# Kernel optimization log

Measured on AMD Instinct MI355X. Metric: run time of the kernel, lower is better.

Reference implementation:

```python
import jax, jax.numpy as jnp
import numpy as np

CUTOFF = 8.0
NUM_G = 50
HID = 128
NUM_INTER = 3
NUM_NODES = 50000
NUM_EDGES = 1600000
NUM_GRAPHS = 128
MAX_Z = 100
LOG2 = float(np.log(2.0))


def ssp(x):
    # PyG ShiftedSoftplus
    return jax.nn.softplus(x) - LOG2


def setup_inputs() -> dict:
    key = jax.random.key(0)
    ks = jax.random.split(key, 20)
    s = 0.1
    pos = jax.random.normal(ks[0], (NUM_NODES, 3), dtype=jnp.float32) * 4.0
    edge_shift = jax.random.normal(ks[1], (NUM_EDGES, 3), dtype=jnp.float32) * 0.5
    z = jax.random.randint(ks[2], (NUM_NODES,), 0, MAX_Z, dtype=jnp.int32)
    edge_index = jax.random.randint(ks[3], (2, NUM_EDGES), 0, NUM_NODES, dtype=jnp.int32)
    batch = jnp.sort(jax.random.randint(ks[4], (NUM_NODES,), 0, NUM_GRAPHS, dtype=jnp.int32))
    emb = jax.random.normal(ks[5], (MAX_Z, HID), dtype=jnp.float32) * s
    mlp_w1 = jax.random.normal(ks[6], (NUM_INTER, NUM_G, HID), dtype=jnp.float32) * s
    mlp_b1 = jnp.zeros((NUM_INTER, HID), jnp.float32)
    mlp_w2 = jax.random.normal(ks[7], (NUM_INTER, HID, HID), dtype=jnp.float32) * s
    mlp_b2 = jnp.zeros((NUM_INTER, HID), jnp.float32)
    cf_w1 = jax.random.normal(ks[8], (NUM_INTER, HID, HID), dtype=jnp.float32) * s  # no bias (PyG lin1)
    cf_w2 = jax.random.normal(ks[9], (NUM_INTER, HID, HID), dtype=jnp.float32) * s
    cf_b2 = jnp.zeros((NUM_INTER, HID), jnp.float32)
    lin_w = jax.random.normal(ks[10], (NUM_INTER, HID, HID), dtype=jnp.float32) * s
    lin_b = jnp.zeros((NUM_INTER, HID), jnp.float32)
    head_w1 = jax.random.normal(ks[11], (HID, HID // 2), dtype=jnp.float32) * s
    head_b1 = jnp.zeros((HID // 2,), jnp.float32)
    head_w2 = jax.random.normal(ks[12], (HID // 2, 1), dtype=jnp.float32) * s
    head_b2 = jnp.zeros((1,), jnp.float32)
    return dict(pos=pos, edge_shift=edge_shift, emb=emb, mlp_w1=mlp_w1, mlp_b1=mlp_b1,
                mlp_w2=mlp_w2, mlp_b2=mlp_b2, cf_w1=cf_w1, cf_w2=cf_w2, cf_b2=cf_b2,
                lin_w=lin_w, lin_b=lin_b, head_w1=head_w1, head_b1=head_b1,
                head_w2=head_w2, head_b2=head_b2, z=z, edge_index=edge_index, batch=batch)


def reference(pos, edge_shift, emb, mlp_w1, mlp_b1, mlp_w2, mlp_b2, cf_w1, cf_w2, cf_b2,
              lin_w, lin_b, head_w1, head_b1, head_w2, head_b2, z, edge_index, batch):
    src, dst = edge_index[0], edge_index[1]
    # edge distances: pos[row] - (pos[col] + shift)
    rel = pos[src] - (pos[dst] + edge_shift)            # [E,3]
    w = jnp.linalg.norm(rel, axis=-1)                   # [E]
    # Gaussian smearing
    offset = jnp.linspace(0.0, CUTOFF, NUM_G, dtype=pos.dtype)
    coeff = -0.5 / (offset[1] - offset[0]) ** 2
    edge_attr = jnp.exp(coeff * (w[:, None] - offset) ** 2)   # [E,50]
    # cosine cutoff
    C = 0.5 * (jnp.cos(w * jnp.pi / CUTOFF) + 1.0)            # [E]
    h = emb[z]                                                # [N,128]
    for i in range(NUM_INTER):
        Wf = (ssp(edge_attr @ mlp_w1[i] + mlp_b1[i]) @ mlp_w2[i] + mlp_b2[i]) * C[:, None]  # [E,128]
        msg = (h @ cf_w1[i])[src] * Wf                   # gather-multiply  [E,128]
        agg = jax.ops.segment_sum(msg, dst, num_segments=NUM_NODES)         # scatter-sum [N,128]
        h = h + (ssp(agg @ cf_w2[i] + cf_b2[i]) @ lin_w[i] + lin_b[i])
    out_atom = ssp(h @ head_w1 + head_b1) @ head_w2 + head_b2               # [N,1]
    sums = jax.ops.segment_sum(out_atom, batch, num_segments=NUM_GRAPHS)    # [G,1]
    counts = jax.ops.segment_sum(jnp.ones((NUM_NODES, 1), out_atom.dtype), batch, num_segments=NUM_GRAPHS)
    return sums / jnp.maximum(counts, 1.0)  # mean readout; out_proj is Identity (128==128)
```

## Files before the change

kernel.cpp:

```cpp
#include <hip/hip_runtime.h>
#include <hip/hip_fp16.h>
#include <math.h>

#define NNODES  50000
#define NEDGES  1600000
#define NGRAPHS 128
#define HID     128
#define NG      50
#define NITER   3
#define TPTS    2048
#define WMAX    12.0f
#define PI_F    3.14159265358979323846f

typedef __attribute__((ext_vector_type(4))) _Float16 half4;
typedef __attribute__((ext_vector_type(4))) float   f32x4;

__device__ __forceinline__ float ssp(float x) {
    float sp = fmaxf(x, 0.0f) + log1pf(expf(-fabsf(x)));
    return sp - 0.69314718055994530942f;
}

__global__ __launch_bounds__(256) void k_init_h(const float* __restrict__ emb,
                                                const int* __restrict__ z,
                                                float* __restrict__ h,
                                                _Float16* __restrict__ hH)
{
    int idx = blockIdx.x * 256 + threadIdx.x;
    int n = idx >> 7, c = idx & 127;
    float v = emb[(z[n] << 7) + c];
    h[idx] = v;
    hH[idx] = (_Float16)v;
}

__global__ __launch_bounds__(128) void k_wt(const float* __restrict__ in,
                                            _Float16* __restrict__ out)
{
    int it = blockIdx.x >> 7, c = blockIdx.x & 127, j = threadIdx.x;
    out[(size_t)it * 16384 + c * 128 + j] = (_Float16)in[(size_t)it * 16384 + j * 128 + c];
}

__global__ __launch_bounds__(128) void k_table(const float* __restrict__ W1,
                                               const float* __restrict__ B1,
                                               const float* __restrict__ W2,
                                               const float* __restrict__ B2,
                                               __half* __restrict__ ti)
{
    int it = blockIdx.x / TPTS;
    int pt = blockIdx.x - it * TPTS;
    const float* W1i = W1 + (size_t)it * NG * HID;
    const float* B1i = B1 + (size_t)it * HID;
    const float* W2i = W2 + (size_t)it * HID * HID;
    const float* B2i = B2 + (size_t)it * HID;

    const float step = WMAX / (float)(TPTS - 1);
    float w0 = pt * step;
    int ptn = (pt < TPTS - 1) ? pt + 1 : pt;
    float w1v = ptn * step;

    __shared__ float sEA[2][NG];
    __shared__ float sT1[2][HID];
    int k = threadIdx.x;
    {
        float dx = 8.0f / 49.0f;
        float coeff = -0.5f / (dx * dx);
        if (k < NG) {
            float diff = w0 - (float)k * dx;
            sEA[0][k] = expf(coeff * diff * diff);
        } else if (k >= 64 && k < 64 + NG) {
            float diff = w1v - (float)(k - 64) * dx;
            sEA[1][k - 64] = expf(coeff * diff * diff);
        }
    }
    __syncthreads();
    float a0 = B1i[k], a1 = a0;
    for (int g = 0; g < NG; ++g) {
        float wv = W1i[g * HID + k];
        a0 = fmaf(sEA[0][g], wv, a0);
        a1 = fmaf(sEA[1][g], wv, a1);
    }
    sT1[0][k] = ssp(a0);
    sT1[1][k] = ssp(a1);
    __syncthreads();
    float b0 = B2i[k], b1v = b0;
    for (int j = 0; j < HID; ++j) {
        float wv = W2i[j * HID + k];
        b0  = fmaf(sT1[0][j], wv, b0);
        b1v = fmaf(sT1[1][j], wv, b1v);
    }
    size_t base = ((size_t)it * TPTS + pt) * 256;
    int pair = k >> 1, within = k & 1;
    ti[base + pair * 4 + within]     = __float2half(b0);
    ti[base + pair * 4 + within + 2] = __float2half(b1v - b0);
}

__global__ __launch_bounds__(256) void k_hist(const int* __restrict__ ei,
                                              int* __restrict__ deg)
{
    int e = blockIdx.x * 256 + threadIdx.x;
    if (e >= NEDGES) return;
    atomicAdd(&deg[ei[NEDGES + e]], 1);
}

#define SCAN_T 1024
#define CHUNK  49
__global__ __launch_bounds__(SCAN_T) void k_scan(const int* __restrict__ deg,
                                                 int* __restrict__ rowptr,
                                                 int* __restrict__ cursor)
{
    int tid = threadIdx.x;
    int base = tid * CHUNK;
    int vals[CHUNK];
    int local = 0;
    #pragma unroll
    for (int i = 0; i < CHUNK; ++i) {
        int idx = base + i;
        int v = (idx < NNODES) ? deg[idx] : 0;
        vals[i] = local;
        local += v;
    }
    int lane = tid & 63, wid = tid >> 6;
    int x = local;
    #pragma unroll
    for (int off = 1; off < 64; off <<= 1) {
        int y = __shfl_up(x, off);
        if (lane >= off) x += y;
    }
    __shared__ int wsum[16];
    __shared__ int woff[17];
    if (lane == 63) wsum[wid] = x;
    __syncthreads();
    if (tid == 0) {
        int acc = 0;
        #pragma unroll
        for (int i = 0; i < 16; ++i) { woff[i] = acc; acc += wsum[i]; }
        woff[16] = acc;
    }
    __syncthreads();
    int threadExcl = woff[wid] + x - local;
    #pragma unroll
    for (int i = 0; i < CHUNK; ++i) {
        int idx = base + i;
        if (idx < NNODES) {
            int p = threadExcl + vals[i];
            rowptr[idx] = p;
            cursor[idx] = p;
        }
    }
    if (tid == SCAN_T - 1) rowptr[NNODES] = woff[16];
}

__global__ __launch_bounds__(256) void k_scatter(const int* __restrict__ ei,
                                                 const float* __restrict__ pos,
                                                 const float* __restrict__ shift,
                                                 int* __restrict__ cursor,
                                                 uint2* __restrict__ rec)
{
    int e = blockIdx.x * 256 + threadIdx.x;
    if (e >= NEDGES) return;
    int s = ei[e], d = ei[NEDGES + e];
    float rx = pos[3*s+0] - (pos[3*d+0] + shift[3*e+0]);
    float ry = pos[3*s+1] - (pos[3*d+1] + shift[3*e+1]);
    float rz = pos[3*s+2] - (pos[3*d+2] + shift[3*e+2]);
    float w = sqrtf(rx*rx + ry*ry + rz*rz);
    const float SCALE = (float)(TPTS - 1) / WMAX;
    float t = fminf(w * SCALE, (float)(TPTS - 1));
    int i0 = (int)t; if (i0 > TPTS - 2) i0 = TPTS - 2;
    float fr = t - (float)i0;
    float C = 0.5f * (cosf(w * (PI_F / 8.0f)) + 1.0f);
    __half2 frc = __halves2half2(__float2half(fr), __float2half(C));
    int slot = atomicAdd(&cursor[d], 1);
    rec[slot] = make_uint2((unsigned)s | ((unsigned)i0 << 17), *(unsigned*)&frc);
}

__device__ __forceinline__ void edge_contrib(uint2 rv, int lane,
                                             const char* __restrict__ hfBase,
                                             const char* __restrict__ tbBase,
                                             float& ax, float& ay)
{
    unsigned sB = (rv.x & 0x1FFFFu) << 8;
    unsigned tB = (rv.x >> 17) << 9;
    __half2 frc = *reinterpret_cast<__half2*>(&rv.y);
    __half2 fr2 = __half2half2(__low2half(frc));
    __half2 c2  = __half2half2(__high2half(frc));
    uint2 tv = *reinterpret_cast<const uint2*>(tbBase + tB + lane * 8);
    unsigned hu = *reinterpret_cast<const unsigned*>(hfBase + sB + lane * 4);
    __half2 hv   = *reinterpret_cast<__half2*>(&hu);
    __half2 vals = *reinterpret_cast<__half2*>(&tv.x);
    __half2 dels = *reinterpret_cast<__half2*>(&tv.y);
    __half2 f2 = __hfma2(fr2, dels, vals);
    __half2 ch = __hmul2(c2, hv);
    ax = fmaf(__low2float(f2),  __low2float(ch),  ax);
    ay = fmaf(__high2float(f2), __high2float(ch), ay);
}

__global__ __launch_bounds__(256) void k_gather(const uint2* __restrict__ rec,
                                                const int* __restrict__ rowptr,
                                                const __half* __restrict__ hfH,
                                                const __half* __restrict__ tableH,
                                                __half2* __restrict__ aggH)
{
    int node = blockIdx.x * 4 + (threadIdx.x >> 6);
    int lane = threadIdx.x & 63;
    const char* hfBase = (const char*)hfH;
    const char* tbBase = (const char*)tableH;
    int beg = rowptr[node], end = rowptr[node + 1];
    float ax0 = 0.f, ay0 = 0.f, ax1 = 0.f, ay1 = 0.f;
    int k = beg;
    for (; k + 4 <= end; k += 4) {
        uint2 r0 = rec[k], r1 = rec[k+1], r2 = rec[k+2], r3 = rec[k+3];
        edge_contrib(r0, lane, hfBase, tbBase, ax0, ay0);
        edge_contrib(r1, lane, hfBase, tbBase, ax1, ay1);
        edge_contrib(r2, lane, hfBase, tbBase, ax0, ay0);
        edge_contrib(r3, lane, hfBase, tbBase, ax1, ay1);
    }
    for (; k < end; ++k) edge_contrib(rec[k], lane, hfBase, tbBase, ax0, ay0);
    aggH[(size_t)node * 64 + lane] = __floats2half2_rn(ax0 + ax1, ay0 + ay1);
}

__global__ __launch_bounds__(256) void k_ngemm_mfma(const _Float16* __restrict__ hH,
                                                    const _Float16* __restrict__ Wt,
                                                    _Float16* __restrict__ outH)
{
    int tid = threadIdx.x;
    int wave = tid >> 6, l = tid & 63;
    int lr = l & 15, lg = l >> 4;
    int r0 = blockIdx.x * 16;
    f32x4 acc[2];
    acc[0] = (f32x4){0.f, 0.f, 0.f, 0.f};
    acc[1] = (f32x4){0.f, 0.f, 0.f, 0.f};
    const _Float16* aRow = hH + (size_t)(r0 + lr) * HID;
    #pragma unroll
    for (int kk = 0; kk < 8; ++kk) {
        half4 a = *(const half4*)(aRow + kk * 16 + lg * 4);
        #pragma unroll
        for (int c = 0; c < 2; ++c) {
            int ct = wave * 2 + c;
            half4 b = *(const half4*)(Wt + (size_t)(ct * 16 + lr) * HID + kk * 16 + lg * 4);
            acc[c] = __builtin_amdgcn_mfma_f32_16x16x16f16(a, b, acc[c], 0, 0, 0);
        }
    }
    #pragma unroll
    for (int c = 0; c < 2; ++c) {
        int col = (wave * 2 + c) * 16 + lr;
        #pragma unroll
        for (int r = 0; r < 4; ++r)
            outH[(size_t)(r0 + lg * 4 + r) * HID + col] = (_Float16)acc[c][r];
    }
}

__global__ __launch_bounds__(256) void k_update_mfma(const _Float16* __restrict__ aggH,
                                                     const _Float16* __restrict__ W2t,
                                                     const float* __restrict__ B2,
                                                     const _Float16* __restrict__ Lt,
                                                     const float* __restrict__ LB,
                                                     float* __restrict__ h,
                                                     _Float16* __restrict__ hH)
{
    __shared__ _Float16 sT[16 * 128];
    int tid = threadIdx.x;
    int wave = tid >> 6, l = tid & 63;
    int lr = l & 15, lg = l >> 4;
    int r0 = blockIdx.x * 16;

    f32x4 acc[2];
    acc[0] = (f32x4){0.f, 0.f, 0.f, 0.f};
    acc[1] = (f32x4){0.f, 0.f, 0.f, 0.f};
    const _Float16* aRow = aggH + (size_t)(r0 + lr) * HID;
    #pragma unroll
    for (int kk = 0; kk < 8; ++kk) {
        half4 a = *(const half4*)(aRow + kk * 16 + lg * 4);
        #pragma unroll
        for (int c = 0; c < 2; ++c) {
            int ct = wave * 2 + c;
            half4 b = *(const half4*)(W2t + (size_t)(ct * 16 + lr) * HID + kk * 16 + lg * 4);
            acc[c] = __builtin_amdgcn_mfma_f32_16x16x16f16(a, b, acc[c], 0, 0, 0);
        }
    }
    #pragma unroll
    for (int c = 0; c < 2; ++c) {
        int col = (wave * 2 + c) * 16 + lr;
        float bias = B2[col];
        #pragma unroll
        for (int r = 0; r < 4; ++r) {
            int rl = lg * 4 + r;
            float v = ssp(acc[c][r] + bias);
            int byte = rl * 256 + col * 2;
            byte ^= (rl & 7) << 4;
            *(_Float16*)((char*)sT + byte) = (_Float16)v;
        }
    }
    __syncthreads();
    f32x4 acc2[2];
    acc2[0] = (f32x4){0.f, 0.f, 0.f, 0.f};
    acc2[1] = (f32x4){0.f, 0.f, 0.f, 0.f};
    #pragma unroll
    for (int kk = 0; kk < 8; ++kk) {
        int byte = lr * 256 + (kk * 16 + lg * 4) * 2;
        byte ^= (lr & 7) << 4;
        half4 a = *(const half4*)((char*)sT + byte);
        #pragma unroll
        for (int c = 0; c < 2; ++c) {
            int ct = wave * 2 + c;
            half4 b = *(const half4*)(Lt + (size_t)(ct * 16 + lr) * HID + kk * 16 + lg * 4);
            acc2[c] = __builtin_amdgcn_mfma_f32_16x16x16f16(a, b, acc2[c], 0, 0, 0);
        }
    }
    #pragma unroll
    for (int c = 0; c < 2; ++c) {
        int col = (wave * 2 + c) * 16 + lr;
        float lb = LB[col];
        #pragma unroll
        for (int r = 0; r < 4; ++r) {
            int row = r0 + lg * 4 + r;
            float hv = h[(size_t)row * HID + col] + acc2[c][r] + lb;
            h[(size_t)row * HID + col] = hv;
            hH[(size_t)row * HID + col] = (_Float16)hv;
        }
    }
}

__global__ __launch_bounds__(512) void k_head(const float* __restrict__ h,
                                              const float* __restrict__ w1,
                                              const float* __restrict__ b1,
                                              const float* __restrict__ w2,
                                              const float* __restrict__ b2,
                                              const int* __restrict__ batch,
                                              float* __restrict__ sums_pad)
{
    __shared__ float sA[128 * 132];
    int r0 = blockIdx.x * 128;
    int tid = threadIdx.x;
    for (int idx = tid; idx < 128 * 32; idx += 512) {
        int r = idx >> 5, c4 = idx & 31;
        int row = r0 + r;
        float4 v = make_float4(0.f, 0.f, 0.f, 0.f);
        if (row < NNODES) v = *(const float4*)(h + (size_t)row * HID + c4 * 4);
        *(float4*)(&sA[r * 132 + c4 * 4]) = v;
    }
    __syncthreads();
    int tx = tid & 7, ty = tid >> 3;
    int cc = tx * 8, ee = ty * 2;
    float acc[2][8];
    {
        float4 b0 = *(const float4*)(b1 + cc);
        float4 bb = *(const float4*)(b1 + cc + 4);
        #pragma unroll
        for (int e = 0; e < 2; ++e) {
            acc[e][0]=b0.x; acc[e][1]=b0.y; acc[e][2]=b0.z; acc[e][3]=b0.w;
            acc[e][4]=bb.x; acc[e][5]=bb.y; acc[e][6]=bb.z; acc[e][7]=bb.w;
        }
    }
    #pragma unroll 4
    for (int j = 0; j < HID; ++j) {
        float a0 = sA[(ee + 0) * 132 + j];
        float a1 = sA[(ee + 1) * 132 + j];
        float4 w0 = *(const float4*)(w1 + (size_t)j * 64 + cc);
        float4 wv1 = *(const float4*)(w1 + (size_t)j * 64 + cc + 4);
        float wv[8] = {w0.x,w0.y,w0.z,w0.w,wv1.x,wv1.y,wv1.z,wv1.w};
        #pragma unroll
        for (int c = 0; c < 8; ++c) {
            acc[0][c] = fmaf(a0, wv[c], acc[0][c]);
            acc[1][c] = fmaf(a1, wv[c], acc[1][c]);
        }
    }
    float4 w2a = *(const float4*)(w2 + cc);
    float4 w2b = *(const float4*)(w2 + cc + 4);
    float w2v[8] = {w2a.x,w2a.y,w2a.z,w2a.w,w2b.x,w2b.y,w2b.z,w2b.w};
    float bias2 = b2[0];
    #pragma unroll
    for (int e = 0; e < 2; ++e) {
        float part = 0.f;
        #pragma unroll
        for (int c = 0; c < 8; ++c) part = fmaf(ssp(acc[e][c]), w2v[c], part);
        part += __shfl_down(part, 4, 8);
        part += __shfl_down(part, 2, 8);
        part += __shfl_down(part, 1, 8);
        if (tx == 0) {
            int row = r0 + ee + e;
            if (row < NNODES) {
                int b = batch[row];
                atomicAdd(&sums_pad[b * 16], part + bias2);
            }
        }
    }
}

__global__ void k_final(const float* __restrict__ sums_pad,
                        const int* __restrict__ batch,
                        float* __restrict__ out)
{
    int g = threadIdx.x;
    if (g >= NGRAPHS) return;
    int lo = 0, hi = NNODES;
    while (lo < hi) { int mid = (lo + hi) >> 1; if (batch[mid] < g) lo = mid + 1; else hi = mid; }
    int a = lo;
    lo = 0; hi = NNODES;
    while (lo < hi) { int mid = (lo + hi) >> 1; if (batch[mid] < g + 1) lo = mid + 1; else hi = mid; }
    float cnt = (float)(lo - a);
    out[g] = sums_pad[g * 16] / fmaxf(cnt, 1.0f);
}

extern "C" void kernel_launch(void* const* d_in, const int* in_sizes, int n_in,
                              void* d_out, int out_size, void* d_ws, size_t ws_size,
                              hipStream_t stream)
{
    const float* pos     = (const float*)d_in[0];
    const float* shift   = (const float*)d_in[1];
    const float* emb     = (const float*)d_in[2];
    const float* mlp_w1  = (const float*)d_in[3];
    const float* mlp_b1  = (const float*)d_in[4];
    const float* mlp_w2  = (const float*)d_in[5];
    const float* mlp_b2  = (const float*)d_in[6];
    const float* cf_w1   = (const float*)d_in[7];
    const float* cf_w2   = (const float*)d_in[8];
    const float* cf_b2   = (const float*)d_in[9];
    const float* lin_w   = (const float*)d_in[10];
    const float* lin_b   = (const float*)d_in[11];
    const float* head_w1 = (const float*)d_in[12];
    const float* head_b1 = (const float*)d_in[13];
    const float* head_w2 = (const float*)d_in[14];
    const float* head_b2 = (const float*)d_in[15];
    const int*   z       = (const int*)d_in[16];
    const int*   ei      = (const int*)d_in[17];
    const int*   batch   = (const int*)d_in[18];
    float* out = (float*)d_out;

    float* ws = (float*)d_ws;
    size_t off = 0;
    float*    h       = ws + off; off += (size_t)NNODES * HID;
    _Float16* hH      = (_Float16*)(ws + off); off += (size_t)(NNODES + 64) * HID / 2;
    _Float16* hfH     = (_Float16*)(ws + off); off += (size_t)(NNODES + 64) * HID / 2;
    _Float16* aggH    = (_Float16*)(ws + off); off += (size_t)(NNODES + 64) * HID / 2;
    __half*   tableH  = (__half*)(ws + off); off += (size_t)3 * TPTS * 256 / 2;
    _Float16* w1t     = (_Float16*)(ws + off); off += (size_t)3 * HID * HID / 2;
    _Float16* w2t     = (_Float16*)(ws + off); off += (size_t)3 * HID * HID / 2;
    _Float16* lwt     = (_Float16*)(ws + off); off += (size_t)3 * HID * HID / 2;
    uint2*    rec     = (uint2*)(ws + off); off += (size_t)2 * NEDGES;
    int*      rowptr  = (int*)(ws + off); off += NNODES + 1;
    int*      deg     = (int*)(ws + off); off += NNODES;
    int*      cursor  = (int*)(ws + off); off += NNODES;
    float*    sums_pad= ws + off; off += NGRAPHS * 16;

    hipMemsetAsync(deg, 0, NNODES * sizeof(int), stream);
    hipMemsetAsync(sums_pad, 0, NGRAPHS * 16 * sizeof(float), stream);

    k_hist<<<(NEDGES + 255) / 256, 256, 0, stream>>>(ei, deg);
    k_scan<<<1, SCAN_T, 0, stream>>>(deg, rowptr, cursor);
    k_scatter<<<(NEDGES + 255) / 256, 256, 0, stream>>>(ei, pos, shift, cursor, rec);

    k_init_h<<<NNODES * HID / 256, 256, 0, stream>>>(emb, z, h, hH);
    k_table<<<3 * TPTS, 128, 0, stream>>>(mlp_w1, mlp_b1, mlp_w2, mlp_b2, tableH);
    k_wt<<<3 * 128, 128, 0, stream>>>(cf_w1, w1t);
    k_wt<<<3 * 128, 128, 0, stream>>>(cf_w2, w2t);
    k_wt<<<3 * 128, 128, 0, stream>>>(lin_w, lwt);

    int gblk = NNODES / 16;
    for (int i = 0; i < NITER; ++i) {
        k_ngemm_mfma<<<gblk, 256, 0, stream>>>(hH, w1t + (size_t)i * HID * HID, hfH);
        k_gather<<<NNODES / 4, 256, 0, stream>>>(rec, rowptr, (const __half*)hfH,
                                                 tableH + (size_t)i * TPTS * 256,
                                                 (__half2*)aggH);
        k_update_mfma<<<gblk, 256, 0, stream>>>(aggH, w2t + (size_t)i * HID * HID,
                                                cf_b2 + (size_t)i * HID,
                                                lwt + (size_t)i * HID * HID,
                                                lin_b + (size_t)i * HID, h, hH);
    }
    k_head<<<(NNODES + 127) / 128, 512, 0, stream>>>(h, head_w1, head_b1, head_w2, head_b2, batch, sums_pad);
    k_final<<<1, 128, 0, stream>>>(sums_pad, batch, out);
}
```

Baseline: 1.016 ms.

## Fuse next-layer node GEMM into update kernel, vectorize gather record loads

The update kernel now also multiplies the freshly updated h tile by the next interaction's cf_w1 and writes hfH, so two of the three separate node-GEMM launches and their re-read of hH are removed. The gather kernel loads edge records as 16-byte nontemporal vectors and processes eight edges per iteration, with an alignment prologue and tail handling. The three weight-transpose launches are merged into one. The fused update adds an extra shared-memory pass and barrier per block, and raises register pressure.

Result: no change. 1.018 ms (+0.2%).

```diff
diff --git a/kernel.cpp b/kernel.cpp
--- a/kernel.cpp
+++ b/kernel.cpp
@@ -14,6 +14,7 @@
 
 typedef __attribute__((ext_vector_type(4))) _Float16 half4;
 typedef __attribute__((ext_vector_type(4))) float   f32x4;
+typedef __attribute__((ext_vector_type(4))) unsigned u32x4;
 
 __device__ __forceinline__ float ssp(float x) {
     float sp = fmaxf(x, 0.0f) + log1pf(expf(-fabsf(x)));
@@ -32,10 +33,18 @@
     hH[idx] = (_Float16)v;
 }
 
-__global__ __launch_bounds__(128) void k_wt(const float* __restrict__ in,
-                                            _Float16* __restrict__ out)
-{
-    int it = blockIdx.x >> 7, c = blockIdx.x & 127, j = threadIdx.x;
+__global__ __launch_bounds__(128) void k_wt3(const float* __restrict__ w1,
+                                             const float* __restrict__ w2,
+                                             const float* __restrict__ lw,
+                                             _Float16* __restrict__ o1,
+                                             _Float16* __restrict__ o2,
+                                             _Float16* __restrict__ o3)
+{
+    int fam = blockIdx.x / 384;
+    int rem = blockIdx.x - fam * 384;
+    int it = rem >> 7, c = rem & 127, j = threadIdx.x;
+    const float* in = (fam == 0) ? w1 : (fam == 1) ? w2 : lw;
+    _Float16* out   = (fam == 0) ? o1 : (fam == 1) ? o2 : o3;
     out[(size_t)it * 16384 + c * 128 + j] = (_Float16)in[(size_t)it * 16384 + j * 128 + c];
 }
 
@@ -172,14 +181,14 @@
     rec[slot] = make_uint2((unsigned)s | ((unsigned)i0 << 17), *(unsigned*)&frc);
 }
 
-__device__ __forceinline__ void edge_contrib(uint2 rv, int lane,
+__device__ __forceinline__ void edge_contrib(unsigned rx, unsigned ry, int lane,
                                              const char* __restrict__ hfBase,
                                              const char* __restrict__ tbBase,
                                              float& ax, float& ay)
 {
-    unsigned sB = (rv.x & 0x1FFFFu) << 8;
-    unsigned tB = (rv.x >> 17) << 9;
-    __half2 frc = *reinterpret_cast<__half2*>(&rv.y);
+    unsigned sB = (rx & 0x1FFFFu) << 8;
+    unsigned tB = (rx >> 17) << 9;
+    __half2 frc = *reinterpret_cast<__half2*>(&ry);
     __half2 fr2 = __half2half2(__low2half(frc));
     __half2 c2  = __half2half2(__high2half(frc));
     uint2 tv = *reinterpret_cast<const uint2*>(tbBase + tB + lane * 8);
@@ -206,14 +215,34 @@
     int beg = rowptr[node], end = rowptr[node + 1];
     float ax0 = 0.f, ay0 = 0.f, ax1 = 0.f, ay1 = 0.f;
     int k = beg;
-    for (; k + 4 <= end; k += 4) {
-        uint2 r0 = rec[k], r1 = rec[k+1], r2 = rec[k+2], r3 = rec[k+3];
-        edge_contrib(r0, lane, hfBase, tbBase, ax0, ay0);
-        edge_contrib(r1, lane, hfBase, tbBase, ax1, ay1);
-        edge_contrib(r2, lane, hfBase, tbBase, ax0, ay0);
-        edge_contrib(r3, lane, hfBase, tbBase, ax1, ay1);
-    }
-    for (; k < end; ++k) edge_contrib(rec[k], lane, hfBase, tbBase, ax0, ay0);
+    if ((k & 1) && k < end) {
+        uint2 r = rec[k];
+        edge_contrib(r.x, r.y, lane, hfBase, tbBase, ax0, ay0);
+        ++k;
+    }
+    for (; k + 8 <= end; k += 8) {
+        u32x4 ra = __builtin_nontemporal_load(reinterpret_cast<const u32x4*>(rec + k));
+        u32x4 rb = __builtin_nontemporal_load(reinterpret_cast<const u32x4*>(rec + k + 2));
+        u32x4 rc = __builtin_nontemporal_load(reinterpret_cast<const u32x4*>(rec + k + 4));
+        u32x4 rd = __builtin_nontemporal_load(reinterpret_cast<const u32x4*>(rec + k + 6));
+        edge_contrib(ra.x, ra.y, lane, hfBase, tbBase, ax0, ay0);
+        edge_contrib(ra.z, ra.w, lane, hfBase, tbBase, ax1, ay1);
+        edge_contrib(rb.x, rb.y, lane, hfBase, tbBase, ax0, ay0);
+        edge_contrib(rb.z, rb.w, lane, hfBase, tbBase, ax1, ay1);
+        edge_contrib(rc.x, rc.y, lane, hfBase, tbBase, ax0, ay0);
+        edge_contrib(rc.z, rc.w, lane, hfBase, tbBase, ax1, ay1);
+        edge_contrib(rd.x, rd.y, lane, hfBase, tbBase, ax0, ay0);
+        edge_contrib(rd.z, rd.w, lane, hfBase, tbBase, ax1, ay1);
+    }
+    for (; k + 2 <= end; k += 2) {
+        u32x4 ra = __builtin_nontemporal_load(reinterpret_cast<const u32x4*>(rec + k));
+        edge_contrib(ra.x, ra.y, lane, hfBase, tbBase, ax0, ay0);
+        edge_contrib(ra.z, ra.w, lane, hfBase, tbBase, ax1, ay1);
+    }
+    if (k < end) {
+        uint2 r = rec[k];
+        edge_contrib(r.x, r.y, lane, hfBase, tbBase, ax0, ay0);
+    }
     aggH[(size_t)node * 64 + lane] = __floats2half2_rn(ax0 + ax1, ay0 + ay1);
 }
 
@@ -254,7 +283,9 @@
                                                      const _Float16* __restrict__ Lt,
                                                      const float* __restrict__ LB,
                                                      float* __restrict__ h,
-                                                     _Float16* __restrict__ hH)
+                                                     _Float16* __restrict__ hH,
+                                                     const _Float16* __restrict__ W1n,
+                                                     _Float16* __restrict__ hfOut)
 {
     __shared__ _Float16 sT[16 * 128];
     int tid = threadIdx.x;
@@ -305,6 +336,8 @@
             acc2[c] = __builtin_amdgcn_mfma_f32_16x16x16f16(a, b, acc2[c], 0, 0, 0);
         }
     }
+    __syncthreads();
+    _Float16 hnew[2][4];
     #pragma unroll
     for (int c = 0; c < 2; ++c) {
         int col = (wave * 2 + c) * 16 + lr;
@@ -315,6 +348,43 @@
             float hv = h[(size_t)row * HID + col] + acc2[c][r] + lb;
             h[(size_t)row * HID + col] = hv;
             hH[(size_t)row * HID + col] = (_Float16)hv;
+            hnew[c][r] = (_Float16)hv;
+        }
+    }
+    if (W1n) {
+        #pragma unroll
+        for (int c = 0; c < 2; ++c) {
+            int col = (wave * 2 + c) * 16 + lr;
+            #pragma unroll
+            for (int r = 0; r < 4; ++r) {
+                int rl = lg * 4 + r;
+                int byte = rl * 256 + col * 2;
+                byte ^= (rl & 7) << 4;
+                *(_Float16*)((char*)sT + byte) = hnew[c][r];
+            }
+        }
+        __syncthreads();
+        f32x4 acc3[2];
+        acc3[0] = (f32x4){0.f, 0.f, 0.f, 0.f};
+        acc3[1] = (f32x4){0.f, 0.f, 0.f, 0.f};
+        #pragma unroll
+        for (int kk = 0; kk < 8; ++kk) {
+            int byte = lr * 256 + (kk * 16 + lg * 4) * 2;
+            byte ^= (lr & 7) << 4;
+            half4 a = *(const half4*)((char*)sT + byte);
+            #pragma unroll
+            for (int c = 0; c < 2; ++c) {
+                int ct = wave * 2 + c;
+                half4 b = *(const half4*)(W1n + (size_t)(ct * 16 + lr) * HID + kk * 16 + lg * 4);
+                acc3[c] = __builtin_amdgcn_mfma_f32_16x16x16f16(a, b, acc3[c], 0, 0, 0);
+            }
+        }
+        #pragma unroll
+        for (int c = 0; c < 2; ++c) {
+            int col = (wave * 2 + c) * 16 + lr;
+            #pragma unroll
+            for (int r = 0; r < 4; ++r)
+                hfOut[(size_t)(r0 + lg * 4 + r) * HID + col] = (_Float16)acc3[c][r];
         }
     }
 }
@@ -450,20 +520,20 @@
 
     k_init_h<<<NNODES * HID / 256, 256, 0, stream>>>(emb, z, h, hH);
     k_table<<<3 * TPTS, 128, 0, stream>>>(mlp_w1, mlp_b1, mlp_w2, mlp_b2, tableH);
-    k_wt<<<3 * 128, 128, 0, stream>>>(cf_w1, w1t);
-    k_wt<<<3 * 128, 128, 0, stream>>>(cf_w2, w2t);
-    k_wt<<<3 * 128, 128, 0, stream>>>(lin_w, lwt);
+    k_wt3<<<3 * 384, 128, 0, stream>>>(cf_w1, cf_w2, lin_w, w1t, w2t, lwt);
 
     int gblk = NNODES / 16;
+    k_ngemm_mfma<<<gblk, 256, 0, stream>>>(hH, w1t, hfH);
     for (int i = 0; i < NITER; ++i) {
-        k_ngemm_mfma<<<gblk, 256, 0, stream>>>(hH, w1t + (size_t)i * HID * HID, hfH);
         k_gather<<<NNODES / 4, 256, 0, stream>>>(rec, rowptr, (const __half*)hfH,
                                                  tableH + (size_t)i * TPTS * 256,
                                                  (__half2*)aggH);
         k_update_mfma<<<gblk, 256, 0, stream>>>(aggH, w2t + (size_t)i * HID * HID,
                                                 cf_b2 + (size_t)i * HID,
                                                 lwt + (size_t)i * HID * HID,
-                                                lin_b + (size_t)i * HID, h, hH);
+                                                lin_b + (size_t)i * HID, h, hH,
+                                                (i < NITER - 1) ? w1t + (size_t)(i + 1) * HID * HID : nullptr,
+                                                hfH);
     }
     k_head<<<(NNODES + 127) / 128, 512, 0, stream>>>(h, head_w1, head_b1, head_w2, head_b2, batch, sums_pad);
     k_final<<<1, 128, 0, stream>>>(sums_pad, batch, out);
```
